# Optimization experiments

Hardware: AMD Instinct MI355X
Metric: run time of the kernel (lower is better)

The kernel has to match this reference:

```python
import jax, jax.numpy as jnp
import numpy as np


def setup_inputs() -> dict:
    V, D, E = 4096, 128, 12288
    key = jax.random.key(0)
    k1, k2, k3 = jax.random.split(key, 3)
    features = jax.random.normal(k1, (V, D), dtype=jnp.float32)
    # random self-loop-free edge list
    v0 = jax.random.randint(k2, (E,), 0, V)
    off = jax.random.randint(k3, (E,), 1, V)
    v1 = (v0 + off) % V
    edges = jnp.stack([v0, v1]).astype(jnp.int32)  # [2, E]
    # manifold-style neighbor matrix: interior edges share 2 faces
    neighbor = (jnp.zeros((V, V), jnp.int32)
                .at[edges[0], edges[1]].set(2)
                .at[edges[1], edges[0]].set(2))
    return {"features": features, "edges": edges, "neighbor": neighbor}


def _collapse(features, edges, neighbor):
    """Greedy heap-order edge collapse. The heap is built once and only popped,
    so pop order == edges sorted by priority ||f[v0]||^2 + ||f[v1]||^2.
    Returns merge matrix A (f_out = A @ f_in), alive vertex mask, final count."""
    V = neighbor.shape[0]
    target = jnp.int32(V // 2)
    pri = jnp.sum(features * features, axis=1)          # [V]
    epri = pri[edges[0]] + pri[edges[1]]                # [E]
    order = jnp.argsort(epri)                           # heappop order (stable ties)
    alive0 = jnp.ones((V,), bool)
    A0 = jnp.eye(V, dtype=jnp.float32)
    cnt0 = jnp.int32(V)

    def step(carry, e):
        alive, n, A, cnt = carry
        v0 = edges[0, e]
        v1 = edges[1, e]
        do = (cnt > target) & alive[v0] & alive[v1] & (n[v0, v1] == 2)
        # merged neighbor row for v0; v1 dies
        r = (n[v0] + n[v1]).at[v0].set(0).at[v1].set(0)
        row0 = jnp.where(do, r, n[v0])
        row1 = jnp.where(do, jnp.zeros_like(r), n[v1])
        n = (n.at[v0, :].set(row0).at[:, v0].set(row0)
              .at[v1, :].set(row1).at[:, v1].set(row1))
        arow = jnp.where(do, 0.5 * (A[v0] + A[v1]), A[v0])
        A = A.at[v0].set(arow)
        alive = alive.at[v1].set(alive[v1] & jnp.logical_not(do))
        cnt = cnt - do.astype(jnp.int32)
        return (alive, n, A, cnt), None

    (alive, n, A, cnt), _ = jax.lax.scan(step, (alive0, neighbor, A0, cnt0), order)
    return A, alive, cnt


def reference(features, edges, neighbor):
    edges = edges.astype(jnp.int32)
    A, alive, cnt = _collapse(features, edges, neighbor)
    # clean_up() compacts removed vertices; under jit we mask dead rows instead
    pooled = (A @ features) * alive[:, None].astype(features.dtype)
    return pooled, alive, cnt
```

## Files before the change

### kernel.cpp

```cpp
#include <hip/hip_runtime.h>
#include <stdint.h>

#define V 4096
#define D 128
#define E 12288
#define NPAD 16384
#define HALF 8192
#define TARGET 2048
#define MAXM (V - TARGET)
#define ROWU32 256

#define WS_N      0u
#define WS_PRI    (V * ROWU32 * 4u)
#define WS_KEYS   (WS_PRI + V * 4u)
#define WS_PK     (WS_KEYS + NPAD * 8u)
#define WS_PAIRS  (WS_PK + E * 4u)
#define WS_MCOUNT (WS_PAIRS + MAXM * 4u)
#define WS_ALIVE  (WS_MCOUNT + 16u)

__device__ __forceinline__ unsigned getf(const uint4& r, int c) {
    unsigned lo = (c & 2) ? r.z : r.x;
    unsigned hi = (c & 2) ? r.w : r.y;
    return (c & 1) ? hi : lo;
}

__global__ void k_scatter(const int* __restrict__ edges, unsigned* __restrict__ n32) {
    int e = blockIdx.x * 256 + threadIdx.x;
    if (e < E) {
        int a = edges[e], b = edges[E + e];
        atomicOr(&n32[a * ROWU32 + (b >> 4)], 2u << ((b & 15) * 2));
        atomicOr(&n32[b * ROWU32 + (a >> 4)], 2u << ((a & 15) * 2));
    }
}

__global__ void k_pri(const float* __restrict__ f, float* __restrict__ pri) {
    int v = blockIdx.x * 256 + threadIdx.x;
    if (v < V) {
        const float* p = f + v * D;
        float r[8];
#pragma unroll
        for (int j = 0; j < 8; j++) r[j] = __fmul_rn(p[j], p[j]);
        for (int i = 8; i < D; i += 8) {
#pragma unroll
            for (int j = 0; j < 8; j++)
                r[j] = __fadd_rn(r[j], __fmul_rn(p[i + j], p[i + j]));
        }
        float s01 = __fadd_rn(r[0], r[1]);
        float s23 = __fadd_rn(r[2], r[3]);
        float s45 = __fadd_rn(r[4], r[5]);
        float s67 = __fadd_rn(r[6], r[7]);
        pri[v] = __fadd_rn(__fadd_rn(s01, s23), __fadd_rn(s45, s67));
    }
}

__global__ void k_keys(const int* __restrict__ edges, const float* __restrict__ pri,
                       unsigned long long* __restrict__ keys) {
    int s = blockIdx.x * 256 + threadIdx.x;
    if (s < NPAD) {
        unsigned long long rec;
        if (s < E) {
            int a = edges[s], b = edges[E + s];
            float k = __fadd_rn(pri[a], pri[b]);
            rec = ((unsigned long long)__float_as_uint(k) << 32) | (unsigned)s;
        } else {
            rec = (0xFFFFFFFFull << 32) | (unsigned)s;
        }
        keys[s] = rec;
    }
}

__launch_bounds__(1024)
__global__ void k_sort2(unsigned long long* __restrict__ keys) {
    __shared__ unsigned long long srt[HALF];
    const int tid = threadIdx.x;
    unsigned long long* base = keys + blockIdx.x * HALF;
    for (int s = tid; s < HALF; s += 1024) srt[s] = base[s];
    __syncthreads();
    for (int k = 2; k <= HALF; k <<= 1) {
        for (int j = k >> 1; j >= 1; j >>= 1) {
            for (int i = tid; i < HALF; i += 1024) {
                int ixj = i ^ j;
                if (ixj > i) {
                    unsigned long long x = srt[i], y = srt[ixj];
                    bool up = ((i & k) == 0);
                    if ((x > y) == up) { srt[i] = y; srt[ixj] = x; }
                }
            }
            __syncthreads();
        }
    }
    for (int s = tid; s < HALF; s += 1024) base[s] = srt[s];
}

__launch_bounds__(64)
__global__ void k_mergepath(const unsigned long long* __restrict__ keys,
                            const int* __restrict__ edges, unsigned* __restrict__ pkG) {
    int t = blockIdx.x * 64 + threadIdx.x;
    if (t >= E / 64) return;
    const unsigned long long* A = keys;
    const unsigned long long* B = keys + HALF;
    int d = t * 64;
    int lo = d > HALF ? d - HALF : 0;
    int hi = d < HALF ? d : HALF;
    while (lo < hi) {
        int mid = (lo + hi) >> 1;
        if (A[mid] < B[d - 1 - mid]) lo = mid + 1; else hi = mid;
    }
    int ia = lo, ib = d - lo;
    for (int o = d; o < d + 64; o++) {
        bool takeA = (ib >= HALF) || (ia < HALF && A[ia] < B[ib]);
        unsigned long long r = takeA ? A[ia++] : B[ib++];
        int e = (int)(r & 0xFFFFFFFFull);
        int a = edges[e], b = edges[E + e];
        pkG[o] = ((unsigned)a << 16) | (unsigned)b;
    }
}

__launch_bounds__(64)
__global__ void k_collapse(const unsigned* __restrict__ pkG, unsigned* n32,
                           unsigned* __restrict__ pairsG, int* __restrict__ mcountG,
                           uint8_t* __restrict__ aliveG, float* __restrict__ out) {
    __shared__ uint8_t alive[V];
    const int lane = threadIdx.x;
    for (int v = lane; v < V; v += 64) alive[v] = 1;
    __syncthreads();

    int cnt = V, mcount = 0;
    bool done = false;

    for (int w = 0; w < E && !done; w += 64) {
        unsigned pkv = pkG[w + lane];
        const int a = (int)(pkv >> 16), b = (int)(pkv & 0xFFFFu);
        const int widx = a * ROWU32 + (b >> 4);
        const int wsh = (b & 15) * 2;
        bool dec = false;

        while (!done) {
            __builtin_amdgcn_s_waitcnt(0);
            bool av = alive[a] && alive[b];
            unsigned wv = ((volatile unsigned*)n32)[widx];
            bool flag = !dec && av && (((wv >> wsh) & 3u) == 2u);
            if (!dec && !av) dec = true;

            bool pois = false, vis = false, accMe = false;
            unsigned long long accMask = 0ull;
            int nacc = 0;
            int limit = cnt - TARGET; if (limit > 8) limit = 8;
            int scanEnd = 64;
            while (true) {
                unsigned long long m = __ballot(!dec && !vis && (flag || pois));
                if (!m) break;
                int i = __ffsll(m) - 1;
                unsigned long long pb = __ballot(pois);
                int ai = __shfl(a, i), bi = __shfl(b, i);
                bool isP = (pb >> i) & 1ull;
                if (!isP) {
                    if (nacc < limit) {
                        accMask |= 1ull << i; nacc++;
                        if (lane == i) { dec = true; accMe = true; }
                    } else { scanEnd = i; break; }
                } else {
                    if (lane == i) vis = true;
                }
                if (lane > i && (a == ai || a == bi || b == ai || b == bi)) pois = true;
            }
            if (!dec && !vis && !pois && !flag && lane < scanEnd) dec = true;

            if (nacc == 0) break;

            uint4 RA[8], RB[8];
            int MV0[8], MV1[8];
            {
                unsigned long long am = accMask;
#pragma unroll
                for (int jj = 0; jj < 8; jj++) {
                    if (jj < nacc) {
                        int lj = __ffsll(am) - 1; am &= am - 1ull;
                        int v0 = __shfl(a, lj), v1 = __shfl(b, lj);
                        MV0[jj] = v0; MV1[jj] = v1;
                        RA[jj] = *((const uint4*)(n32 + v0 * ROWU32) + lane);
                        RB[jj] = *((const uint4*)(n32 + v1 * ROWU32) + lane);
                    }
                }
            }

            unsigned keptMask = 0;
            uint4 RBU = make_uint4(0u, 0u, 0u, 0u);
#pragma unroll
            for (int jj = 0; jj < 8; jj++) {
                if (jj < nacc) {
                    int v0 = MV0[jj], v1 = MV1[jj];
                    bool c = false;
                    if ((v0 >> 6) == lane)
                        c |= ((getf(RBU, (v0 >> 4) & 3) >> ((v0 & 15) * 2)) & 3u) != 0u;
                    if ((v1 >> 6) == lane)
                        c |= ((getf(RBU, (v1 >> 4) & 3) >> ((v1 & 15) * 2)) & 3u) != 0u;
                    if (__ballot(c) == 0ull) {
                        keptMask |= 1u << jj;
                        RBU.x |= RB[jj].x; RBU.y |= RB[jj].y;
                        RBU.z |= RB[jj].z; RBU.w |= RB[jj].w;
                    }
                }
            }
            if (accMe) {
                int myjj = (int)__popcll(accMask & ((1ull << lane) - 1ull));
                if (!((keptMask >> myjj) & 1u)) dec = false;
            }

#pragma unroll
            for (int jj = 0; jj < 8; jj++) {
                if (jj < nacc && ((keptMask >> jj) & 1u)) {
                    int v0 = MV0[jj], v1 = MV1[jj];
                    uint4 ra = RA[jj], rb = RB[jj];
                    uint4 rr;
                    rr.x = ra.x | rb.x | ((ra.x & rb.x & 0xAAAAAAAAu) >> 1);
                    rr.y = ra.y | rb.y | ((ra.y & rb.y & 0xAAAAAAAAu) >> 1);
                    rr.z = ra.z | rb.z | ((ra.z & rb.z & 0xAAAAAAAAu) >> 1);
                    rr.w = ra.w | rb.w | ((ra.w & rb.w & 0xAAAAAAAAu) >> 1);
                    if ((v0 >> 6) == lane) {
                        unsigned msk = ~(3u << ((v0 & 15) * 2)); int c = (v0 >> 4) & 3;
                        if (c == 0) rr.x &= msk; else if (c == 1) rr.y &= msk;
                        else if (c == 2) rr.z &= msk; else rr.w &= msk;
                    }
                    if ((v1 >> 6) == lane) {
                        unsigned msk = ~(3u << ((v1 & 15) * 2)); int c = (v1 >> 4) & 3;
                        if (c == 0) rr.x &= msk; else if (c == 1) rr.y &= msk;
                        else if (c == 2) rr.z &= msk; else rr.w &= msk;
                    }
                    *((uint4*)(n32 + v0 * ROWU32) + lane) = rr;
                    int sh0 = (v0 & 15) * 2;
                    int wi0 = v0 >> 4;
#pragma unroll
                    for (int c = 0; c < 4; c++) {
                        unsigned bb = getf(rb, c);
                        if (!bb) continue;
                        unsigned aa = getf(ra, c);
                        unsigned vv = getf(rr, c);
                        int xbase = (lane << 6) + (c << 4);
                        unsigned t = bb;
                        while (t) {
                            int q = (__ffs(t) - 1) >> 1;
                            t &= ~(3u << (q * 2));
                            int x = xbase + q;
                            if (x != v0 && x != v1) {
                                unsigned o0  = (aa >> (q * 2)) & 3u;
                                unsigned val = (vv >> (q * 2)) & 3u;
                                unsigned dx = (o0 ^ val) << sh0;
                                if (dx) atomicXor(n32 + x * ROWU32 + wi0, dx);
                            }
                        }
                    }
                    if (lane == 0) {
                        alive[v1] = 0;
                        pairsG[mcount] = ((unsigned)v0 << 16) | (unsigned)v1;
                    }
                    mcount++; cnt--;
                }
            }
            if (cnt == TARGET) done = true;
            if (__ballot(!dec) == 0ull) break;
        }
    }

    __builtin_amdgcn_s_waitcnt(0);
    for (int v = lane; v < V; v += 64) {
        uint8_t ao = alive[v];
        aliveG[v] = ao;
        out[V * D + v] = ao ? 1.0f : 0.0f;
    }
    if (lane == 0) { mcountG[0] = mcount; out[V * D + V] = (float)cnt; }
}

__launch_bounds__(256)
__global__ void k_apply(const float* __restrict__ f, const unsigned* __restrict__ pairsG,
                        const int* __restrict__ mcountG, float* __restrict__ out) {
    __shared__ unsigned pl[MAXM];
    __shared__ int rootL[256];
    __shared__ float wL[256];
    const int tid = threadIdx.x;
    const int mc = mcountG[0];
    for (int j = tid; j < mc; j += 256) pl[j] = pairsG[j];
    __syncthreads();
    int cur = blockIdx.x * 256 + tid;
    float w = 1.0f;
    for (int j = 0; j < mc; j++) {
        unsigned p = pl[j];
        int v0 = (int)(p >> 16), v1 = (int)(p & 0xFFFFu);
        if (cur == v1) { cur = v0; w *= 0.5f; }
        else if (cur == v0) w *= 0.5f;
    }
    rootL[tid] = cur;
    wL[tid] = w;
    __syncthreads();
    const int sub = tid >> 7;
    const int d = tid & 127;
    for (int s = 0; s < 256; s += 2) {
        int idx = s + sub;
        int vv = blockIdx.x * 256 + idx;
        atomicAdd(&out[rootL[idx] * D + d], wL[idx] * f[vv * D + d]);
    }
}

extern "C" void kernel_launch(void* const* d_in, const int* in_sizes, int n_in,
                              void* d_out, int out_size, void* d_ws, size_t ws_size,
                              hipStream_t stream) {
    (void)in_sizes; (void)n_in; (void)out_size; (void)ws_size;
    const float* features = (const float*)d_in[0];
    const int* edges = (const int*)d_in[1];
    uint8_t* ws = (uint8_t*)d_ws;
    unsigned* n32 = (unsigned*)(ws + WS_N);
    float* pri = (float*)(ws + WS_PRI);
    unsigned long long* keys = (unsigned long long*)(ws + WS_KEYS);
    unsigned* pkG = (unsigned*)(ws + WS_PK);
    unsigned* pairsG = (unsigned*)(ws + WS_PAIRS);
    int* mcountG = (int*)(ws + WS_MCOUNT);
    uint8_t* aliveG = ws + WS_ALIVE;
    float* out = (float*)d_out;

    hipMemsetAsync(n32, 0, (size_t)V * ROWU32 * 4, stream);
    hipMemsetAsync(out, 0, (size_t)V * D * sizeof(float), stream);
    k_pri<<<(V + 255) / 256, 256, 0, stream>>>(features, pri);
    k_scatter<<<(E + 255) / 256, 256, 0, stream>>>(edges, n32);
    k_keys<<<(NPAD + 255) / 256, 256, 0, stream>>>(edges, pri, keys);
    k_sort2<<<2, 1024, 0, stream>>>(keys);
    k_mergepath<<<(E / 64 + 63) / 64, 64, 0, stream>>>(keys, edges, pkG);
    k_collapse<<<1, 64, 0, stream>>>(pkG, n32, pairsG, mcountG, aliveG, out);
    k_apply<<<V / 256, 256, 0, stream>>>(features, pairsG, mcountG, out);
}
```

Baseline: 3.482 ms.

## Batch up to 16 collapses per round with hashed conflict detection and LDS flag updates

The sequential collapse loop now picks up to 16 candidate edges per round instead of 8. Candidate conflicts are found with a 64-bit hashed vertex bitmask rather than a serial ballot/shuffle scan. Each edge's neighbor flag is refreshed from merged rows cached in shared memory instead of re-reading global memory every round, and the per-round alive reload and full waitcnt are removed. The aim is fewer serialized rounds and less global-memory latency on the single-wave critical path. The cost is more register pressure from 16 row pairs and subtler correctness conditions for the poison and cutoff logic, since hash collisions can cause spurious conflicts.

```diff
diff --git a/kernel.cpp b/kernel.cpp
--- a/kernel.cpp
+++ b/kernel.cpp
@@ -9,6 +9,10 @@
 #define TARGET 2048
 #define MAXM (V - TARGET)
 #define ROWU32 256
+#define CAP 16
+
+#define WAIT_VM0   0x0F70
+#define WAIT_LGKM0 0xC07F
 
 #define WS_N      0u
 #define WS_PRI    (V * ROWU32 * 4u)
@@ -116,126 +120,137 @@
     }
 }
 
-__launch_bounds__(64)
+__launch_bounds__(64, 1)
 __global__ void k_collapse(const unsigned* __restrict__ pkG, unsigned* n32,
                            unsigned* __restrict__ pairsG, int* __restrict__ mcountG,
                            uint8_t* __restrict__ aliveG, float* __restrict__ out) {
+    __shared__ unsigned shPk[64];
+    __shared__ unsigned shRR[CAP * ROWU32];
     __shared__ uint8_t alive[V];
     const int lane = threadIdx.x;
     for (int v = lane; v < V; v += 64) alive[v] = 1;
-    __syncthreads();
+    __builtin_amdgcn_s_waitcnt(WAIT_LGKM0);
 
     int cnt = V, mcount = 0;
     bool done = false;
 
     for (int w = 0; w < E && !done; w += 64) {
+        __builtin_amdgcn_s_waitcnt(WAIT_VM0);
         unsigned pkv = pkG[w + lane];
         const int a = (int)(pkv >> 16), b = (int)(pkv & 0xFFFFu);
-        const int widx = a * ROWU32 + (b >> 4);
-        const int wsh = (b & 15) * 2;
+        shPk[lane] = pkv;
+        unsigned wv = *(volatile unsigned*)(n32 + a * ROWU32 + (b >> 4));
+        unsigned fv = (wv >> ((b & 15) * 2)) & 3u;
+        __builtin_amdgcn_s_waitcnt(WAIT_LGKM0);
+        bool av = alive[a] && alive[b];
         bool dec = false;
 
-        while (!done) {
-            __builtin_amdgcn_s_waitcnt(0);
-            bool av = alive[a] && alive[b];
-            unsigned wv = ((volatile unsigned*)n32)[widx];
-            bool flag = !dec && av && (((wv >> wsh) & 3u) == 2u);
-            if (!dec && !av) dec = true;
-
-            bool pois = false, vis = false, accMe = false;
-            unsigned long long accMask = 0ull;
-            int nacc = 0;
-            int limit = cnt - TARGET; if (limit > 8) limit = 8;
-            int scanEnd = 64;
-            while (true) {
-                unsigned long long m = __ballot(!dec && !vis && (flag || pois));
-                if (!m) break;
-                int i = __ffsll(m) - 1;
-                unsigned long long pb = __ballot(pois);
-                int ai = __shfl(a, i), bi = __shfl(b, i);
-                bool isP = (pb >> i) & 1ull;
-                if (!isP) {
-                    if (nacc < limit) {
-                        accMask |= 1ull << i; nacc++;
-                        if (lane == i) { dec = true; accMe = true; }
-                    } else { scanEnd = i; break; }
-                } else {
-                    if (lane == i) vis = true;
-                }
-                if (lane > i && (a == ai || a == bi || b == ai || b == bi)) pois = true;
-            }
-            if (!dec && !vis && !pois && !flag && lane < scanEnd) dec = true;
-
-            if (nacc == 0) break;
-
-            uint4 RA[8], RB[8];
-            int MV0[8], MV1[8];
-            {
-                unsigned long long am = accMask;
-#pragma unroll
-                for (int jj = 0; jj < 8; jj++) {
-                    if (jj < nacc) {
-                        int lj = __ffsll(am) - 1; am &= am - 1ull;
-                        int v0 = __shfl(a, lj), v1 = __shfl(b, lj);
-                        MV0[jj] = v0; MV1[jj] = v1;
-                        RA[jj] = *((const uint4*)(n32 + v0 * ROWU32) + lane);
-                        RB[jj] = *((const uint4*)(n32 + v1 * ROWU32) + lane);
-                    }
-                }
-            }
-
-            unsigned keptMask = 0;
+        for (int rnd = 0; rnd < 96 && !done; rnd++) {
+            bool flag = !dec && av && (fv == 2u);
+            unsigned long long mF = __ballot(flag);
+            if (!mF) break;
+            int limit = cnt - TARGET; if (limit > CAP) limit = CAP;
+
+            unsigned candPk[CAP]; int candLane[CAP];
+            int F = 0;
+            unsigned long long mIt = mF;
+#pragma unroll
+            for (int k = 0; k < CAP; k++) {
+                int i = -1; unsigned cp = 0u;
+                if (mIt) { i = __ffsll(mIt) - 1; mIt &= mIt - 1ull; F = k + 1; cp = shPk[i]; }
+                candLane[k] = i; candPk[k] = cp;
+            }
+            int cutoff = mIt ? (__ffsll(mIt) - 1) : 64;
+
+            unsigned long long B = 0ull;
+            unsigned accBits = 0u; int nacc = 0;
+            bool myPois = false; int myK = -1;
+#pragma unroll
+            for (int k = 0; k < CAP; k++) {
+                if (k < F) {
+                    int i = candLane[k];
+                    if (nacc >= limit) { if (i < cutoff) cutoff = i; }
+                    else {
+                        int pa = (int)(candPk[k] >> 16), pb = (int)(candPk[k] & 0xFFFFu);
+                        unsigned long long bits = (1ull << ((pa ^ (pa >> 6)) & 63)) |
+                                                  (1ull << ((pb ^ (pb >> 6)) & 63));
+                        bool conf = (B & bits) != 0ull;
+                        if (!conf) { accBits |= 1u << k; nacc++; if (lane == i) myK = k; }
+                        B |= bits;
+                        if (i < lane && (pa == a || pa == b || pb == a || pb == b))
+                            myPois = true;
+                    }
+                }
+            }
+            if (!dec && !flag && !myPois && lane < cutoff) dec = true;
+
+            __builtin_amdgcn_s_waitcnt(WAIT_VM0);
+            uint4 RA[CAP], RB[CAP];
+#pragma unroll
+            for (int k = 0; k < CAP; k++) {
+                if ((accBits >> k) & 1u) {
+                    int v0 = (int)(candPk[k] >> 16), v1 = (int)(candPk[k] & 0xFFFFu);
+                    RA[k] = *((const uint4*)(n32 + v0 * ROWU32) + lane);
+                    RB[k] = *((const uint4*)(n32 + v1 * ROWU32) + lane);
+                }
+            }
+
+            unsigned keptBits = 0u;
             uint4 RBU = make_uint4(0u, 0u, 0u, 0u);
-#pragma unroll
-            for (int jj = 0; jj < 8; jj++) {
-                if (jj < nacc) {
-                    int v0 = MV0[jj], v1 = MV1[jj];
+            uint4 MV0 = make_uint4(0u, 0u, 0u, 0u);
+#pragma unroll
+            for (int k = 0; k < CAP; k++) {
+                if ((accBits >> k) & 1u) {
+                    int v0 = (int)(candPk[k] >> 16), v1 = (int)(candPk[k] & 0xFFFFu);
                     bool c = false;
                     if ((v0 >> 6) == lane)
                         c |= ((getf(RBU, (v0 >> 4) & 3) >> ((v0 & 15) * 2)) & 3u) != 0u;
                     if ((v1 >> 6) == lane)
                         c |= ((getf(RBU, (v1 >> 4) & 3) >> ((v1 & 15) * 2)) & 3u) != 0u;
+                    c |= ((RB[k].x & MV0.x) | (RB[k].y & MV0.y) |
+                          (RB[k].z & MV0.z) | (RB[k].w & MV0.w)) != 0u;
                     if (__ballot(c) == 0ull) {
-                        keptMask |= 1u << jj;
-                        RBU.x |= RB[jj].x; RBU.y |= RB[jj].y;
-                        RBU.z |= RB[jj].z; RBU.w |= RB[jj].w;
-                    }
-                }
-            }
-            if (accMe) {
-                int myjj = (int)__popcll(accMask & ((1ull << lane) - 1ull));
-                if (!((keptMask >> myjj) & 1u)) dec = false;
-            }
-
-#pragma unroll
-            for (int jj = 0; jj < 8; jj++) {
-                if (jj < nacc && ((keptMask >> jj) & 1u)) {
-                    int v0 = MV0[jj], v1 = MV1[jj];
-                    uint4 ra = RA[jj], rb = RB[jj];
+                        keptBits |= 1u << k;
+                        RBU.x |= RB[k].x; RBU.y |= RB[k].y;
+                        RBU.z |= RB[k].z; RBU.w |= RB[k].w;
+                        if ((v0 >> 6) == lane) {
+                            int c4 = (v0 >> 4) & 3; unsigned bit = 3u << ((v0 & 15) * 2);
+                            if (c4 == 0) MV0.x |= bit; else if (c4 == 1) MV0.y |= bit;
+                            else if (c4 == 2) MV0.z |= bit; else MV0.w |= bit;
+                        }
+                    }
+                }
+            }
+            if (myK >= 0 && ((keptBits >> myK) & 1u)) dec = true;
+
+#pragma unroll
+            for (int k = 0; k < CAP; k++) {
+                if ((keptBits >> k) & 1u) {
+                    int v0 = (int)(candPk[k] >> 16), v1 = (int)(candPk[k] & 0xFFFFu);
+                    uint4 ra = RA[k], rb = RB[k];
                     uint4 rr;
                     rr.x = ra.x | rb.x | ((ra.x & rb.x & 0xAAAAAAAAu) >> 1);
                     rr.y = ra.y | rb.y | ((ra.y & rb.y & 0xAAAAAAAAu) >> 1);
                     rr.z = ra.z | rb.z | ((ra.z & rb.z & 0xAAAAAAAAu) >> 1);
                     rr.w = ra.w | rb.w | ((ra.w & rb.w & 0xAAAAAAAAu) >> 1);
                     if ((v0 >> 6) == lane) {
-                        unsigned msk = ~(3u << ((v0 & 15) * 2)); int c = (v0 >> 4) & 3;
-                        if (c == 0) rr.x &= msk; else if (c == 1) rr.y &= msk;
-                        else if (c == 2) rr.z &= msk; else rr.w &= msk;
+                        int c4 = (v0 >> 4) & 3; unsigned m = ~(3u << ((v0 & 15) * 2));
+                        if (c4 == 0) rr.x &= m; else if (c4 == 1) rr.y &= m;
+                        else if (c4 == 2) rr.z &= m; else rr.w &= m;
                     }
                     if ((v1 >> 6) == lane) {
-                        unsigned msk = ~(3u << ((v1 & 15) * 2)); int c = (v1 >> 4) & 3;
-                        if (c == 0) rr.x &= msk; else if (c == 1) rr.y &= msk;
-                        else if (c == 2) rr.z &= msk; else rr.w &= msk;
+                        int c4 = (v1 >> 4) & 3; unsigned m = ~(3u << ((v1 & 15) * 2));
+                        if (c4 == 0) rr.x &= m; else if (c4 == 1) rr.y &= m;
+                        else if (c4 == 2) rr.z &= m; else rr.w &= m;
                     }
                     *((uint4*)(n32 + v0 * ROWU32) + lane) = rr;
-                    int sh0 = (v0 & 15) * 2;
-                    int wi0 = v0 >> 4;
+                    *((uint4*)(shRR + k * ROWU32) + lane) = rr;
+                    int sh0 = (v0 & 15) * 2, wi0 = v0 >> 4;
 #pragma unroll
                     for (int c = 0; c < 4; c++) {
                         unsigned bb = getf(rb, c);
                         if (!bb) continue;
-                        unsigned aa = getf(ra, c);
-                        unsigned vv = getf(rr, c);
+                        unsigned aa = getf(ra, c), vv = getf(rr, c);
                         int xbase = (lane << 6) + (c << 4);
                         unsigned t = bb;
                         while (t) {
@@ -243,9 +258,7 @@
                             t &= ~(3u << (q * 2));
                             int x = xbase + q;
                             if (x != v0 && x != v1) {
-                                unsigned o0  = (aa >> (q * 2)) & 3u;
-                                unsigned val = (vv >> (q * 2)) & 3u;
-                                unsigned dx = (o0 ^ val) << sh0;
+                                unsigned dx = (((aa >> (q * 2)) ^ (vv >> (q * 2))) & 3u) << sh0;
                                 if (dx) atomicXor(n32 + x * ROWU32 + wi0, dx);
                             }
                         }
@@ -257,12 +270,25 @@
                     mcount++; cnt--;
                 }
             }
+            __builtin_amdgcn_s_waitcnt(WAIT_LGKM0);
+
+            int ja = -1, jb = -1;
+#pragma unroll
+            for (int k = 0; k < CAP; k++) {
+                if ((keptBits >> k) & 1u) {
+                    int v0 = (int)(candPk[k] >> 16), v1 = (int)(candPk[k] & 0xFFFFu);
+                    if (a == v1 || b == v1) dec = true;
+                    if (a == v0) ja = k;
+                    if (b == v0) jb = k;
+                }
+            }
+            if (jb >= 0)      fv = (shRR[jb * ROWU32 + (a >> 4)] >> ((a & 15) * 2)) & 3u;
+            else if (ja >= 0) fv = (shRR[ja * ROWU32 + (b >> 4)] >> ((b & 15) * 2)) & 3u;
+
             if (cnt == TARGET) done = true;
-            if (__ballot(!dec) == 0ull) break;
         }
     }
 
-    __builtin_amdgcn_s_waitcnt(0);
     for (int v = lane; v < V; v += 64) {
         uint8_t ao = alive[v];
         aliveG[v] = ao;
```

Result: slower. 3.875 ms (+11.3%).
